# Optimization experiments

Hardware: AMD Instinct MI355X
Metric: run time of the kernel (lower is better)

Reference implementation:

```python
import jax, jax.numpy as jnp
import numpy as np
from jax import lax

DIST_THRESH = 180.0
ATT_THRESH = 0.05


def setup_inputs() -> dict:
    key = jax.random.key(0)
    ks = jax.random.split(key, 6)
    B, N, H, W = 16, 512, 25, 25
    F, Fh = H * W, int(H * W * 1.5)  # 625, 937
    x4 = jax.random.normal(ks[0], (B, N, H, W), dtype=jnp.float32) * 0.25
    attention = jax.random.uniform(ks[1], (B, N, 1, 1), dtype=jnp.float32)
    W1 = jax.random.normal(ks[2], (2, F, Fh), dtype=jnp.float32) * (1.0 / np.sqrt(F))
    b1 = jnp.zeros((Fh,), dtype=jnp.float32)
    W2 = jax.random.normal(ks[3], (2, Fh, F), dtype=jnp.float32) * (1.0 / np.sqrt(Fh))
    b2 = jnp.zeros((F,), dtype=jnp.float32)
    return {"x4": x4, "attention": attention, "W1": W1, "b1": b1, "W2": W2, "b2": b2}


def _build_adjacency(X, att):
    """X: [B,N,F] node features, att: [B,N]. Returns thresholded adjacency [B,N,N]."""
    B, N, F = X.shape
    # pairwise L1 distances, row-by-row scan to avoid materializing [B,N,N,F]
    Xs = jnp.swapaxes(X, 0, 1)  # [N,B,F]

    def row(_, xi):  # xi: [B,F]
        d = jnp.sum(jnp.abs(xi[:, None, :] - X), axis=-1)  # [B,N]
        return None, d

    _, D = lax.scan(row, None, Xs)          # [N,B,N]
    D = jnp.swapaxes(D, 0, 1)               # [B,N,N]
    att_d = jnp.abs(att[:, :, None] - att[:, None, :])  # [B,N,N]
    A = ((D <= DIST_THRESH) & (att_d <= ATT_THRESH)).astype(jnp.float32)
    # original only fills i<j and j<i, diagonal stays 0
    A = A * (1.0 - jnp.eye(N, dtype=jnp.float32))
    return A


def _process_graph(A):
    """A + I, then row-normalize by inverse degree (D^-1 (A+I))."""
    N = A.shape[1]
    A = A + jnp.eye(N, dtype=A.dtype)
    deg = jnp.sum(A, axis=-1)               # [B,N]
    dinv = jnp.where(deg > 0, 1.0 / deg, 0.0)
    return dinv[:, :, None] * A


def _cheb_conv(x, L, Wk, b):
    """ChebConv with K=2 over dense normalized graph L: T0=x, T1=Lx."""
    t1 = jnp.einsum('bij,bjf->bif', L, x)
    return jnp.einsum('bnf,fo->bno', x, Wk[0]) + jnp.einsum('bnf,fo->bno', t1, Wk[1]) + b


def reference(x4, attention, W1, b1, W2, b2):
    B, N, H, W = x4.shape
    X = x4.reshape(B, N, H * W)             # [B,N,625] flow_x
    att = attention[:, :, 0, 0]             # [B,N]
    A = _build_adjacency(X, att)
    L = _process_graph(A)
    h = jax.nn.relu(_cheb_conv(X, L, W1, b1))   # [B,N,937]
    out = jax.nn.relu(_cheb_conv(h, L, W2, b2))  # [B,N,625]
    return out
```

## Files before the change

### kernel.cpp

```cpp
#include <hip/hip_runtime.h>
#include <stdint.h>

typedef uint16_t u16;
typedef uint32_t u32;
typedef __attribute__((ext_vector_type(4))) float f32x4;
typedef __attribute__((ext_vector_type(4))) unsigned short us4;
typedef __attribute__((ext_vector_type(8))) unsigned short us8;

#define NB   16
#define NN   512
#define FF   625
#define FH   937
#define ROWS 8192
#define KS1  1280
#define KS2  1920
#define NPX  640
#define NPH  960
#define F4   160

using frag_ab = __attribute__((ext_vector_type(8))) short;
using frag_cd = __attribute__((ext_vector_type(4))) float;

__device__ __forceinline__ u16 f32_bf16(float f) {
  union { float f; uint32_t u; } x; x.f = f;
  uint32_t r = x.u + 0x7fffu + ((x.u >> 16) & 1u);
  return (u16)(r >> 16);
}
__device__ __forceinline__ void gload_lds16(const void* g, void* l) {
  __builtin_amdgcn_global_load_lds((__attribute__((address_space(1))) void*)g,
                                   (__attribute__((address_space(3))) void*)l,
                                   16, 0, 0);
}
__device__ __forceinline__ int swiz_row(int blk) {
  return ((blk & 7) << 10) | (blk >> 3);
}

__global__ __launch_bounds__(256) void prep(
    const float* __restrict__ x4, const float* __restrict__ W1,
    const float* __restrict__ W2, f32x4* __restrict__ Xpad,
    u16* __restrict__ Xcat, u16* __restrict__ Xt,
    u16* __restrict__ W1t, u16* __restrict__ W2t)
{
  const int blk = blockIdx.x;
  const int tid = threadIdx.x;
  if (blk < 4096) {
    const int xcd = blk & 7, loc = blk >> 3;
    const int row0 = xcd * 1024 + loc * 2;
    for (int s = tid; s < 320; s += 256) {
      const int row = row0 + (s >= 160);
      const int k4 = (s >= 160) ? s - 160 : s;
      f32x4 v; us4 o;
      #pragma unroll
      for (int t = 0; t < 4; ++t) {
        const int f = k4 * 4 + t;
        float x = (f < FF) ? x4[(size_t)row * FF + f] : 0.f;
        v[t] = x; o[t] = f32_bf16(x);
      }
      Xpad[(size_t)row * F4 + k4] = v;
      *(us4*)(Xcat + (size_t)row * KS1 + k4 * 4) = o;
    }
  } else if (blk < 9216) {
    __shared__ float tile[32][33];
    const int bb = blk - 4096;
    const int xcd = bb & 7, sub = bb >> 3;
    const int b = xcd * 2 + sub / 320;
    const int t = sub % 320;
    const int ft = t % 20, kt = t / 20;
    const int tx = tid & 31, ty = tid >> 5;
    #pragma unroll
    for (int r = 0; r < 4; ++r) {
      const int node = kt * 32 + ty + r * 8;
      const int f = ft * 32 + tx;
      tile[ty + r * 8][tx] = (f < FF) ? x4[((size_t)b * NN + node) * FF + f] : 0.f;
    }
    __syncthreads();
    #pragma unroll
    for (int r = 0; r < 4; ++r) {
      const int f = ft * 32 + ty + r * 8;
      const int node = kt * 32 + tx;
      Xt[((size_t)b * NPX + f) * 512 + node] = f32_bf16(tile[tx][ty + r * 8]);
    }
  } else if (blk < 10496) {
    __shared__ float tile[32][33];
    const int bb = blk - 9216;
    const int kt = bb % 40, nt = bb / 40;
    const int tx = tid & 31, ty = tid >> 5;
    #pragma unroll
    for (int r = 0; r < 4; ++r) {
      int k = kt * 32 + ty + r * 8;
      int n = nt * 32 + tx;
      float v = 0.f;
      int c = -1, kk = 0;
      if (k < 625) { c = 0; kk = k; }
      else if (k >= 640 && k < 1265) { c = 1; kk = k - 640; }
      if (c >= 0 && n < FH) v = W1[((size_t)c * 625 + kk) * FH + n];
      tile[ty + r * 8][tx] = v;
    }
    __syncthreads();
    #pragma unroll
    for (int r = 0; r < 4; ++r) {
      int n = nt * 32 + ty + r * 8;
      int k = kt * 32 + tx;
      W1t[(size_t)n * KS1 + k] = f32_bf16(tile[tx][ty + r * 8]);
    }
  } else {
    __shared__ float tile[32][33];
    const int bb = blk - 10496;
    const int kt = bb % 60, nt = bb / 60;
    const int tx = tid & 31, ty = tid >> 5;
    #pragma unroll
    for (int r = 0; r < 4; ++r) {
      int k = kt * 32 + ty + r * 8;
      int n = nt * 32 + tx;
      float v = 0.f;
      int c = -1, kk = 0;
      if (k < 937) { c = 0; kk = k; }
      else if (k >= 960 && k < 1897) { c = 1; kk = k - 960; }
      if (c >= 0 && n < FF) v = W2[((size_t)c * 937 + kk) * FF + n];
      tile[ty + r * 8][tx] = v;
    }
    __syncthreads();
    #pragma unroll
    for (int r = 0; r < 4; ++r) {
      int n = nt * 32 + ty + r * 8;
      int k = kt * 32 + tx;
      W2t[(size_t)n * KS2 + k] = f32_bf16(tile[tx][ty + r * 8]);
    }
  }
}

__global__ __launch_bounds__(256) void build_L(
    const f32x4* __restrict__ Xpad,
    const float* __restrict__ att,
    u16* __restrict__ L)
{
  __shared__ float att_sh[512];
  __shared__ f32x4 Xi4[F4];
  __shared__ u16 cand[512];
  __shared__ u16 flag[512];
  __shared__ int ncand, nacc;

  const int tid = threadIdx.x;
  const int row = swiz_row(blockIdx.x);
  const int b = row >> 9;
  const int i = row & 511;
  const f32x4* Xb4 = Xpad + (size_t)b * NN * F4;

  att_sh[tid]       = att[b * NN + tid];
  att_sh[tid + 256] = att[b * NN + tid + 256];
  if (tid < F4) Xi4[tid] = Xb4[(size_t)i * F4 + tid];
  flag[tid] = 0; flag[tid + 256] = 0;
  if (tid == 0) { ncand = 0; nacc = 0; }
  __syncthreads();

  const float ai = att_sh[i];
  for (int j = tid; j < NN; j += 256) {
    if (j != i && fabsf(ai - att_sh[j]) <= 0.05f) {
      int p = atomicAdd(&ncand, 1);
      cand[p] = (u16)j;
    }
  }
  __syncthreads();
  if (tid == 0) flag[i] = 1;

  const int hl = tid & 31;
  const int hw = tid >> 5;
  const int nc = ncand;

  const f32x4 a0 = Xi4[hl];
  const f32x4 a1 = Xi4[32 + hl];
  const f32x4 a2 = Xi4[64 + hl];
  const f32x4 a3 = Xi4[96 + hl];
  const f32x4 a4 = Xi4[128 + hl];

  for (int c = hw; c < nc; c += 8) {
    const int j = cand[c];
    const f32x4* Xj = Xb4 + (size_t)j * F4;
    const f32x4 d0 = a0 - Xj[hl];
    const f32x4 d1 = a1 - Xj[32 + hl];
    const f32x4 d2 = a2 - Xj[64 + hl];
    const f32x4 d3 = a3 - Xj[96 + hl];
    const f32x4 d4 = a4 - Xj[128 + hl];
    float p = 0.f;
    #pragma unroll
    for (int t = 0; t < 4; ++t)
      p += fabsf(d0[t]) + fabsf(d1[t]) + fabsf(d2[t]) + fabsf(d3[t]) + fabsf(d4[t]);
    #pragma unroll
    for (int off = 16; off; off >>= 1) p += __shfl_xor(p, off, 64);
    if (hl == 0 && p <= 180.0f) {
      atomicAdd(&nacc, 1);
      flag[j] = 1;
    }
  }
  __syncthreads();

  const u16 dv = f32_bf16(1.0f / (float)(nacc + 1));
  const u32 lo = flag[2 * tid]     ? (u32)dv : 0u;
  const u32 hi = flag[2 * tid + 1] ? (u32)dv : 0u;
  *(u32*)(L + (size_t)row * 512 + 2 * tid) = lo | (hi << 16);
}

template <int KS, int NTILE, int NREAL, int NSTORE, bool RELU, bool BIAS, bool OUT_BF16>
__device__ __forceinline__ void gemm_core(
    const u16* __restrict__ At,
    const u16* __restrict__ Btt,
    const float* __restrict__ bias, void* __restrict__ C,
    long crow0, int col0, int ldc)
{
  constexpr int NI = NTILE / 32;
  constexpr int BR = NTILE / 32;
  __shared__ __align__(16) u16 Ash[128 * 64];
  __shared__ __align__(16) u16 Bsh[NTILE * 64];

  const int tid  = threadIdx.x;
  const int lane = tid & 63;
  const int wave = tid >> 6;
  const int wm = wave & 1, wn = wave >> 1;
  const int q = lane >> 4, l16 = lane & 15;

  const u16* pa[4]; const u16* pb[BR];
  #pragma unroll
  for (int r = 0; r < 4; ++r) {
    const int ci = r * 256 + tid;
    const int row = ci >> 3, cpos = ci & 7;
    pa[r] = At + (size_t)row * KS + (cpos ^ (row & 7)) * 8;
  }
  #pragma unroll
  for (int r = 0; r < BR; ++r) {
    const int ci = r * 256 + tid;
    const int row = ci >> 3, cpos = ci & 7;
    pb[r] = Btt + (size_t)row * KS + (cpos ^ (row & 7)) * 8;
  }
  const int wbase = (tid & 192) * 8;

  const frag_ab* fA[4][2]; const frag_ab* fB[NI][2];
  #pragma unroll
  for (int mi = 0; mi < 4; ++mi) {
    const int row = wm * 64 + mi * 16 + l16;
    fA[mi][0] = (const frag_ab*)&Ash[row * 64 + ((q    ) ^ (l16 & 7)) * 8];
    fA[mi][1] = (const frag_ab*)&Ash[row * 64 + ((q + 4) ^ (l16 & 7)) * 8];
  }
  #pragma unroll
  for (int ni = 0; ni < NI; ++ni) {
    const int row = wn * (NTILE / 2) + ni * 16 + l16;
    fB[ni][0] = (const frag_ab*)&Bsh[row * 64 + ((q    ) ^ (l16 & 7)) * 8];
    fB[ni][1] = (const frag_ab*)&Bsh[row * 64 + ((q + 4) ^ (l16 & 7)) * 8];
  }

  frag_cd acc[4][NI] = {};

  constexpr int KT = KS / 64;
  for (int kt = 0; kt < KT; ++kt) {
    __syncthreads();
    #pragma unroll
    for (int r = 0; r < 4; ++r) { gload_lds16(pa[r], &Ash[r * 2048 + wbase]); pa[r] += 64; }
    #pragma unroll
    for (int r = 0; r < BR; ++r) { gload_lds16(pb[r], &Bsh[r * 2048 + wbase]); pb[r] += 64; }
    __syncthreads();

    #pragma unroll
    for (int kk = 0; kk < 2; ++kk) {
      frag_ab av[4], bv[NI];
      #pragma unroll
      for (int mi = 0; mi < 4; ++mi) av[mi] = *fA[mi][kk];
      #pragma unroll
      for (int ni = 0; ni < NI; ++ni) bv[ni] = *fB[ni][kk];
      #pragma unroll
      for (int mi = 0; mi < 4; ++mi)
        #pragma unroll
        for (int ni = 0; ni < NI; ++ni)
          acc[mi][ni] = __builtin_amdgcn_mfma_f32_16x16x32_bf16(
              av[mi], bv[ni], acc[mi][ni], 0, 0, 0);
    }
  }

  #pragma unroll
  for (int ni = 0; ni < NI; ++ni) {
    const int col = col0 + wn * (NTILE / 2) + ni * 16 + l16;
    if (col >= NSTORE) continue;
    const bool ok = (col < NREAL);
    float bvv = 0.f;
    if (BIAS) bvv = ok ? bias[col] : 0.f;
    #pragma unroll
    for (int mi = 0; mi < 4; ++mi) {
      #pragma unroll
      for (int r = 0; r < 4; ++r) {
        const long rowg = crow0 + wm * 64 + mi * 16 + q * 4 + r;
        float v = acc[mi][ni][r];
        if (BIAS) v += bvv;
        if (RELU) v = fmaxf(v, 0.f);
        if (!ok) v = 0.f;
        if (OUT_BF16) ((u16*)C)[rowg * (size_t)ldc + col] = f32_bf16(v);
        else          ((float*)C)[rowg * (size_t)ldc + col] = v;
      }
    }
  }
}

template <int KS, int NTILE, int NREAL, int NSTORE, bool RELU, bool BIAS, bool OUT_BF16>
__global__ __launch_bounds__(256) void gemm_dense(
    const u16* __restrict__ A, const u16* __restrict__ Bt,
    const float* __restrict__ bias, void* __restrict__ C, int ldc)
{
  const int x = blockIdx.x;
  const int mt = ((x & 7) << 3) | (x >> 3);
  gemm_core<KS, NTILE, NREAL, NSTORE, RELU, BIAS, OUT_BF16>(
      A + (size_t)mt * 128 * KS, Bt + (size_t)blockIdx.y * NTILE * KS,
      bias, C, (long)mt * 128, blockIdx.y * NTILE, ldc);
}

template <int NP>
__global__ __launch_bounds__(256) void spmm(
    const u16* __restrict__ L, const u16* __restrict__ Bt,
    u16* __restrict__ C, int ldc)
{
  constexpr int TPB = 4 * (NP / 64);
  const int blk = blockIdx.x;
  const int xcd = blk & 7, sub = blk >> 3;
  const int b = xcd * 2 + sub / TPB;
  const int t = sub % TPB;
  const int mt = t & 3, nt = t >> 2;
  gemm_core<512, 64, NP, NP, false, false, true>(
      L + ((size_t)b * 512 + mt * 128) * 512,
      Bt + ((size_t)b * NP + nt * 64) * 512,
      nullptr, C, (long)b * 512 + mt * 128, nt * 64, ldc);
}

__global__ __launch_bounds__(256) void transpose_h(
    const u16* __restrict__ hcat, u16* __restrict__ ht)
{
  __shared__ u16 tile[32][34];
  const int blk = blockIdx.x;
  const int xcd = blk & 7, sub = blk >> 3;
  const int b = xcd * 2 + sub / 480;
  const int t = sub % 480;
  const int kt = t % 16, nt = t / 16;
  const int tid = threadIdx.x;
  const int tx = tid & 31, ty = tid >> 5;
  #pragma unroll
  for (int r = 0; r < 4; ++r) {
    const int node = kt * 32 + ty + r * 8;
    const int n = nt * 32 + tx;
    tile[ty + r * 8][tx] = hcat[((size_t)b * NN + node) * KS2 + n];
  }
  __syncthreads();
  #pragma unroll
  for (int r = 0; r < 4; ++r) {
    const int n = nt * 32 + ty + r * 8;
    const int node = kt * 32 + tx;
    ht[((size_t)b * NPH + n) * 512 + node] = tile[tx][ty + r * 8];
  }
}

extern "C" void kernel_launch(void* const* d_in, const int* in_sizes, int n_in,
                              void* d_out, int out_size, void* d_ws, size_t ws_size,
                              hipStream_t stream) {
  const float* x4  = (const float*)d_in[0];
  const float* att = (const float*)d_in[1];
  const float* W1  = (const float*)d_in[2];
  const float* b1  = (const float*)d_in[3];
  const float* W2  = (const float*)d_in[4];
  const float* b2  = (const float*)d_in[5];
  float* out = (float*)d_out;

  char* ws = (char*)d_ws;
  f32x4* Xpad = (f32x4*)ws;
  u16* ht = (u16*)ws;       ws += (size_t)ROWS * F4 * 16;
  u16* Xcat = (u16*)ws;  ws += (size_t)ROWS * KS1 * 2;
  u16* hcat = (u16*)ws;  ws += (size_t)ROWS * KS2 * 2;
  u16* W1t  = (u16*)ws;  ws += (size_t)1024 * KS1 * 2;
  u16* W2t  = (u16*)ws;  ws += (size_t)640 * KS2 * 2;
  u16* Lm   = (u16*)ws;  ws += (size_t)NB * 512 * 512 * 2;
  u16* Xt   = (u16*)ws;  ws += (size_t)NB * NPX * 512 * 2;

  prep<<<dim3(11696), 256, 0, stream>>>(x4, W1, W2, Xpad, Xcat, Xt, W1t, W2t);
  build_L<<<dim3(ROWS), 256, 0, stream>>>(Xpad, att, Lm);
  spmm<NPX><<<dim3(640), 256, 0, stream>>>(Lm, Xt, Xcat + NPX, KS1);
  gemm_dense<KS1, 128, FH, NPH, true, true, true><<<dim3(64, 8), 256, 0, stream>>>(
      Xcat, W1t, b1, (void*)hcat, KS2);
  transpose_h<<<dim3(7680), 256, 0, stream>>>(hcat, ht);
  spmm<NPH><<<dim3(960), 256, 0, stream>>>(Lm, ht, hcat + NPH, KS2);
  gemm_dense<KS2, 64, FF, FF, true, true, false><<<dim3(64, 10), 256, 0, stream>>>(
      hcat, W2t, b2, (void*)out, FF);
}
```

Measured before the change: 222.2 us.

## Sort nodes by attention to tile adjacency build; fuse h transpose into GEMM epilogue

Adds a bitonic sort of attention values per batch inside prep. The new adjacency kernel then processes 8 sorted rows per block, using binary search to restrict candidates to the attention window and reusing each loaded X_j across the 8 rows. L is now zeroed with a memset and filled by sparse scatter writes. The separate transpose kernel for h is removed; the first dense GEMM writes a transposed bf16 copy directly in its epilogue, trading a kernel launch and extra read pass for strided scattered stores.

```diff
diff --git a/kernel.cpp b/kernel.cpp
--- a/kernel.cpp
+++ b/kernel.cpp
@@ -17,6 +17,7 @@
 #define NPX  640
 #define NPH  960
 #define F4   160
+#define ITILE 8
 
 using frag_ab = __attribute__((ext_vector_type(8))) short;
 using frag_cd = __attribute__((ext_vector_type(4))) float;
@@ -31,15 +32,13 @@
                                    (__attribute__((address_space(3))) void*)l,
                                    16, 0, 0);
 }
-__device__ __forceinline__ int swiz_row(int blk) {
-  return ((blk & 7) << 10) | (blk >> 3);
-}
 
 __global__ __launch_bounds__(256) void prep(
-    const float* __restrict__ x4, const float* __restrict__ W1,
-    const float* __restrict__ W2, f32x4* __restrict__ Xpad,
-    u16* __restrict__ Xcat, u16* __restrict__ Xt,
-    u16* __restrict__ W1t, u16* __restrict__ W2t)
+    const float* __restrict__ x4, const float* __restrict__ att,
+    const float* __restrict__ W1, const float* __restrict__ W2,
+    f32x4* __restrict__ Xpad, u16* __restrict__ Xcat, u16* __restrict__ Xt,
+    u16* __restrict__ W1t, u16* __restrict__ W2t,
+    float* __restrict__ att_s, u16* __restrict__ ord_g)
 {
   const int blk = blockIdx.x;
   const int tid = threadIdx.x;
@@ -103,7 +102,7 @@
       int k = kt * 32 + tx;
       W1t[(size_t)n * KS1 + k] = f32_bf16(tile[tx][ty + r * 8]);
     }
-  } else {
+  } else if (blk < 11696) {
     __shared__ float tile[32][33];
     const int bb = blk - 10496;
     const int kt = bb % 60, nt = bb / 60;
@@ -126,86 +125,135 @@
       int k = kt * 32 + tx;
       W2t[(size_t)n * KS2 + k] = f32_bf16(tile[tx][ty + r * 8]);
     }
-  }
-}
-
-__global__ __launch_bounds__(256) void build_L(
+  } else {
+    __shared__ float sa[512];
+    __shared__ u16 so[512];
+    const int b = blk - 11696;
+    sa[tid] = att[b * NN + tid]; sa[tid + 256] = att[b * NN + tid + 256];
+    so[tid] = (u16)tid; so[tid + 256] = (u16)(tid + 256);
+    for (int k = 2; k <= 512; k <<= 1) {
+      for (int j = k >> 1; j > 0; j >>= 1) {
+        __syncthreads();
+        const int i = ((tid & ~(j - 1)) << 1) | (tid & (j - 1));
+        const int p = i | j;
+        const bool up = ((i & k) == 0);
+        const float va = sa[i], vp = sa[p];
+        if ((va > vp) == up) {
+          sa[i] = vp; sa[p] = va;
+          const u16 t = so[i]; so[i] = so[p]; so[p] = t;
+        }
+      }
+    }
+    __syncthreads();
+    att_s[b * NN + tid] = sa[tid]; att_s[b * NN + tid + 256] = sa[tid + 256];
+    ord_g[b * NN + tid] = so[tid]; ord_g[b * NN + tid + 256] = so[tid + 256];
+  }
+}
+
+__global__ __launch_bounds__(256) void build_L_tiled(
     const f32x4* __restrict__ Xpad,
-    const float* __restrict__ att,
+    const float* __restrict__ att_s, const u16* __restrict__ ord_g,
     u16* __restrict__ L)
 {
-  __shared__ float att_sh[512];
-  __shared__ f32x4 Xi4[F4];
-  __shared__ u16 cand[512];
-  __shared__ u16 flag[512];
-  __shared__ int ncand, nacc;
+  __shared__ f32x4 Xi[ITILE][F4];
+  __shared__ float as_[512];
+  __shared__ u16 ord[512];
+  __shared__ u32 mask[ITILE][16];
+  __shared__ int deg[ITILE];
+  __shared__ int jlo_s, jhi_s;
+  __shared__ u16 dvs[ITILE];
 
   const int tid = threadIdx.x;
-  const int row = swiz_row(blockIdx.x);
-  const int b = row >> 9;
-  const int i = row & 511;
+  const int blk = blockIdx.x;
+  const int xcd = blk & 7, sub = blk >> 3;
+  const int b = xcd * 2 + (sub >> 6);
+  const int it = sub & 63;
+  const int s0 = it * ITILE;
   const f32x4* Xb4 = Xpad + (size_t)b * NN * F4;
 
-  att_sh[tid]       = att[b * NN + tid];
-  att_sh[tid + 256] = att[b * NN + tid + 256];
-  if (tid < F4) Xi4[tid] = Xb4[(size_t)i * F4 + tid];
-  flag[tid] = 0; flag[tid + 256] = 0;
-  if (tid == 0) { ncand = 0; nacc = 0; }
+  as_[tid] = att_s[b * NN + tid]; as_[tid + 256] = att_s[b * NN + tid + 256];
+  ord[tid] = ord_g[b * NN + tid]; ord[tid + 256] = ord_g[b * NN + tid + 256];
+  if (tid < ITILE * 16) ((u32*)mask)[tid] = 0;
+  if (tid < ITILE) deg[tid] = 0;
   __syncthreads();
 
-  const float ai = att_sh[i];
-  for (int j = tid; j < NN; j += 256) {
-    if (j != i && fabsf(ai - att_sh[j]) <= 0.05f) {
-      int p = atomicAdd(&ncand, 1);
-      cand[p] = (u16)j;
-    }
+  for (int s = tid; s < ITILE * F4; s += 256) {
+    const int ii = s / F4, k4 = s - ii * F4;
+    Xi[ii][k4] = Xb4[(size_t)ord[s0 + ii] * F4 + k4];
+  }
+  if (tid == 0) {
+    const float lot = as_[s0] - 0.05f;
+    int lo = 0, hi = 512;
+    while (lo < hi) { int m = (lo + hi) >> 1; if (as_[m] < lot) lo = m + 1; else hi = m; }
+    jlo_s = lo;
+  } else if (tid == 1) {
+    const float hit = as_[s0 + ITILE - 1] + 0.05f;
+    int lo = 0, hi = 512;
+    while (lo < hi) { int m = (lo + hi) >> 1; if (as_[m] <= hit) lo = m + 1; else hi = m; }
+    jhi_s = lo;
   }
   __syncthreads();
-  if (tid == 0) flag[i] = 1;
 
   const int hl = tid & 31;
   const int hw = tid >> 5;
-  const int nc = ncand;
-
-  const f32x4 a0 = Xi4[hl];
-  const f32x4 a1 = Xi4[32 + hl];
-  const f32x4 a2 = Xi4[64 + hl];
-  const f32x4 a3 = Xi4[96 + hl];
-  const f32x4 a4 = Xi4[128 + hl];
-
-  for (int c = hw; c < nc; c += 8) {
-    const int j = cand[c];
-    const f32x4* Xj = Xb4 + (size_t)j * F4;
-    const f32x4 d0 = a0 - Xj[hl];
-    const f32x4 d1 = a1 - Xj[32 + hl];
-    const f32x4 d2 = a2 - Xj[64 + hl];
-    const f32x4 d3 = a3 - Xj[96 + hl];
-    const f32x4 d4 = a4 - Xj[128 + hl];
-    float p = 0.f;
-    #pragma unroll
-    for (int t = 0; t < 4; ++t)
-      p += fabsf(d0[t]) + fabsf(d1[t]) + fabsf(d2[t]) + fabsf(d3[t]) + fabsf(d4[t]);
-    #pragma unroll
-    for (int off = 16; off; off >>= 1) p += __shfl_xor(p, off, 64);
-    if (hl == 0 && p <= 180.0f) {
-      atomicAdd(&nacc, 1);
-      flag[j] = 1;
+  const int jlo = jlo_s, jhi = jhi_s;
+
+  for (int sj = jlo + hw; sj < jhi; sj += 8) {
+    const int oj = ord[sj];
+    const f32x4* Xj = Xb4 + (size_t)oj * F4;
+    const f32x4 xj0 = Xj[hl];
+    const f32x4 xj1 = Xj[32 + hl];
+    const f32x4 xj2 = Xj[64 + hl];
+    const f32x4 xj3 = Xj[96 + hl];
+    const f32x4 xj4 = Xj[128 + hl];
+    const float aj = as_[sj];
+    #pragma unroll 2
+    for (int ii = 0; ii < ITILE; ++ii) {
+      const int si = s0 + ii;
+      if (si == sj || fabsf(aj - as_[si]) > 0.05f) continue;
+      const f32x4 d0 = Xi[ii][hl] - xj0;
+      const f32x4 d1 = Xi[ii][32 + hl] - xj1;
+      const f32x4 d2 = Xi[ii][64 + hl] - xj2;
+      const f32x4 d3 = Xi[ii][96 + hl] - xj3;
+      const f32x4 d4 = Xi[ii][128 + hl] - xj4;
+      float p = 0.f;
+      #pragma unroll
+      for (int t = 0; t < 4; ++t)
+        p += fabsf(d0[t]) + fabsf(d1[t]) + fabsf(d2[t]) + fabsf(d3[t]) + fabsf(d4[t]);
+      #pragma unroll
+      for (int off = 16; off; off >>= 1) p += __shfl_xor(p, off, 64);
+      if (hl == 0 && p <= 180.0f) {
+        atomicOr(&mask[ii][sj >> 5], 1u << (sj & 31));
+        atomicAdd(&deg[ii], 1);
+      }
     }
   }
   __syncthreads();
 
-  const u16 dv = f32_bf16(1.0f / (float)(nacc + 1));
-  const u32 lo = flag[2 * tid]     ? (u32)dv : 0u;
-  const u32 hi = flag[2 * tid + 1] ? (u32)dv : 0u;
-  *(u32*)(L + (size_t)row * 512 + 2 * tid) = lo | (hi << 16);
-}
-
-template <int KS, int NTILE, int NREAL, int NSTORE, bool RELU, bool BIAS, bool OUT_BF16>
+  if (tid < ITILE) dvs[tid] = f32_bf16(1.0f / (float)(deg[tid] + 1));
+  __syncthreads();
+
+  if (tid < ITILE * 16) {
+    const int ii = tid >> 4, w = tid & 15;
+    const int oi = ord[s0 + ii];
+    u16* Lrow = L + ((size_t)b * 512 + oi) * 512;
+    const u16 dv = dvs[ii];
+    u32 m = mask[ii][w];
+    while (m) {
+      const int bit = __ffs(m) - 1;
+      m &= m - 1;
+      Lrow[ord[w * 32 + bit]] = dv;
+    }
+    if (w == 0) Lrow[oi] = dv;
+  }
+}
+
+template <int KS, int NTILE, int NREAL, int NSTORE, bool RELU, bool BIAS,
+          bool OUT_BF16, bool TSTORE>
 __device__ __forceinline__ void gemm_core(
-    const u16* __restrict__ At,
-    const u16* __restrict__ Btt,
+    const u16* __restrict__ At, const u16* __restrict__ Btt,
     const float* __restrict__ bias, void* __restrict__ C,
-    long crow0, int col0, int ldc)
+    u16* __restrict__ tbuf, long crow0, int col0, int ldc)
 {
   constexpr int NI = NTILE / 32;
   constexpr int BR = NTILE / 32;
@@ -292,21 +340,26 @@
         if (!ok) v = 0.f;
         if (OUT_BF16) ((u16*)C)[rowg * (size_t)ldc + col] = f32_bf16(v);
         else          ((float*)C)[rowg * (size_t)ldc + col] = v;
+        if (TSTORE) {
+          tbuf[((size_t)(rowg >> 9) * NPH + col) * 512 + (rowg & 511)] = f32_bf16(v);
+        }
       }
     }
   }
 }
 
-template <int KS, int NTILE, int NREAL, int NSTORE, bool RELU, bool BIAS, bool OUT_BF16>
+template <int KS, int NTILE, int NREAL, int NSTORE, bool RELU, bool BIAS,
+          bool OUT_BF16, bool TSTORE>
 __global__ __launch_bounds__(256) void gemm_dense(
     const u16* __restrict__ A, const u16* __restrict__ Bt,
-    const float* __restrict__ bias, void* __restrict__ C, int ldc)
+    const float* __restrict__ bias, void* __restrict__ C,
+    u16* __restrict__ tbuf, int ldc)
 {
   const int x = blockIdx.x;
   const int mt = ((x & 7) << 3) | (x >> 3);
-  gemm_core<KS, NTILE, NREAL, NSTORE, RELU, BIAS, OUT_BF16>(
+  gemm_core<KS, NTILE, NREAL, NSTORE, RELU, BIAS, OUT_BF16, TSTORE>(
       A + (size_t)mt * 128 * KS, Bt + (size_t)blockIdx.y * NTILE * KS,
-      bias, C, (long)mt * 128, blockIdx.y * NTILE, ldc);
+      bias, C, tbuf, (long)mt * 128, blockIdx.y * NTILE, ldc);
 }
 
 template <int NP>
@@ -320,36 +373,10 @@
   const int b = xcd * 2 + sub / TPB;
   const int t = sub % TPB;
   const int mt = t & 3, nt = t >> 2;
-  gemm_core<512, 64, NP, NP, false, false, true>(
+  gemm_core<512, 64, NP, NP, false, false, true, false>(
       L + ((size_t)b * 512 + mt * 128) * 512,
       Bt + ((size_t)b * NP + nt * 64) * 512,
-      nullptr, C, (long)b * 512 + mt * 128, nt * 64, ldc);
-}
-
-__global__ __launch_bounds__(256) void transpose_h(
-    const u16* __restrict__ hcat, u16* __restrict__ ht)
-{
-  __shared__ u16 tile[32][34];
-  const int blk = blockIdx.x;
-  const int xcd = blk & 7, sub = blk >> 3;
-  const int b = xcd * 2 + sub / 480;
-  const int t = sub % 480;
-  const int kt = t % 16, nt = t / 16;
-  const int tid = threadIdx.x;
-  const int tx = tid & 31, ty = tid >> 5;
-  #pragma unroll
-  for (int r = 0; r < 4; ++r) {
-    const int node = kt * 32 + ty + r * 8;
-    const int n = nt * 32 + tx;
-    tile[ty + r * 8][tx] = hcat[((size_t)b * NN + node) * KS2 + n];
-  }
-  __syncthreads();
-  #pragma unroll
-  for (int r = 0; r < 4; ++r) {
-    const int n = nt * 32 + ty + r * 8;
-    const int node = kt * 32 + tx;
-    ht[((size_t)b * NPH + n) * 512 + node] = tile[tx][ty + r * 8];
-  }
+      nullptr, C, nullptr, (long)b * 512 + mt * 128, nt * 64, ldc);
 }
 
 extern "C" void kernel_launch(void* const* d_in, const int* in_sizes, int n_in,
@@ -372,14 +399,17 @@
   u16* W2t  = (u16*)ws;  ws += (size_t)640 * KS2 * 2;
   u16* Lm   = (u16*)ws;  ws += (size_t)NB * 512 * 512 * 2;
   u16* Xt   = (u16*)ws;  ws += (size_t)NB * NPX * 512 * 2;
-
-  prep<<<dim3(11696), 256, 0, stream>>>(x4, W1, W2, Xpad, Xcat, Xt, W1t, W2t);
-  build_L<<<dim3(ROWS), 256, 0, stream>>>(Xpad, att, Lm);
+  float* att_s = (float*)ws; ws += (size_t)NB * NN * 4;
+  u16* ord_g   = (u16*)ws;   ws += (size_t)NB * NN * 2;
+
+  prep<<<dim3(11712), 256, 0, stream>>>(x4, att, W1, W2, Xpad, Xcat, Xt,
+                                        W1t, W2t, att_s, ord_g);
+  hipMemsetAsync(Lm, 0, (size_t)NB * 512 * 512 * 2, stream);
+  build_L_tiled<<<dim3(1024), 256, 0, stream>>>(Xpad, att_s, ord_g, Lm);
   spmm<NPX><<<dim3(640), 256, 0, stream>>>(Lm, Xt, Xcat + NPX, KS1);
-  gemm_dense<KS1, 128, FH, NPH, true, true, true><<<dim3(64, 8), 256, 0, stream>>>(
-      Xcat, W1t, b1, (void*)hcat, KS2);
-  transpose_h<<<dim3(7680), 256, 0, stream>>>(hcat, ht);
+  gemm_dense<KS1, 128, FH, NPH, true, true, true, true>
+      <<<dim3(64, 8), 256, 0, stream>>>(Xcat, W1t, b1, (void*)hcat, ht, KS2);
   spmm<NPH><<<dim3(960), 256, 0, stream>>>(Lm, ht, hcat + NPH, KS2);
-  gemm_dense<KS2, 64, FF, FF, true, true, false><<<dim3(64, 10), 256, 0, stream>>>(
-      hcat, W2t, b2, (void*)out, FF);
-}
+  gemm_dense<KS2, 64, FF, FF, true, true, false, false>
+      <<<dim3(64, 10), 256, 0, stream>>>(hcat, W2t, b2, (void*)out, nullptr, FF);
+}
```

After: 238.0 us. 1.07x slower.
